# Optimization experiments

Hardware: AMD Instinct MI355X
Metric: run time of the kernel (lower is better)

The kernel has to match this reference:

```python
import jax, jax.numpy as jnp
import numpy as np

B, N, DIM, H = 8, 1024, 1024, 8
HEAD_DIM = DIM // H
SCALE = HEAD_DIM ** -0.5  # scale_with_head=True


def setup_inputs() -> dict:
    key = jax.random.key(0)
    k1, k2, k3, k4 = jax.random.split(key, 4)
    return {
        "q": jax.random.normal(k1, (B, N, DIM), dtype=jnp.float32),
        "k": jax.random.normal(k2, (B, N, DIM), dtype=jnp.float32),
        "v": jax.random.normal(k3, (B, N, DIM), dtype=jnp.float32),
        "W_out": jax.random.normal(k4, (DIM, DIM), dtype=jnp.float32) * (DIM ** -0.5),
        "b_out": jnp.zeros((DIM,), dtype=jnp.float32),
    }


def reference(q, k, v, W_out, b_out):
    b, n, dim = q.shape
    h, d = H, dim // H
    # b n (h d) -> b h n d
    def split_heads(t):
        return t.reshape(b, n, h, d).transpose(0, 2, 1, 3)
    qh, kh, vh = split_heads(q), split_heads(k), split_heads(v)
    dots = jnp.einsum('bhid,bhjd->bhij', qh, kh) * SCALE
    attn = jax.nn.softmax(dots, axis=-1)
    out = jnp.einsum('bhij,bhjd->bhid', attn, vh)
    out = out.transpose(0, 2, 1, 3).reshape(b, n, dim)  # b h n d -> b n (h d)
    out = out @ W_out.T + b_out  # nn.Linear(dim, dim); dropout p=0 is identity
    return out, attn
```

## Files before the change

kernel.cpp:

```cpp
#include <hip/hip_runtime.h>

typedef __bf16 bf16x8 __attribute__((ext_vector_type(8)));
typedef unsigned short u16x8 __attribute__((ext_vector_type(8)));
typedef unsigned short u16x4 __attribute__((ext_vector_type(4)));
typedef float f32x4 __attribute__((ext_vector_type(4)));
typedef float f32x16 __attribute__((ext_vector_type(16)));

#define B_    8
#define N_    1024
#define DIM_  1024
#define H_    8
#define HD_   128
#define SCALE_ 0.08838834764831845f

__device__ __forceinline__ unsigned short f2bf(float x) {
  unsigned int u = __float_as_uint(x);
  u += 0x7fffu + ((u >> 16) & 1u);
  return (unsigned short)(u >> 16);
}
__device__ __forceinline__ float bf2f(unsigned short h) {
  return __uint_as_float(((unsigned int)h) << 16);
}
__device__ __forceinline__ f32x4 mfma16(u16x8 a, u16x8 b, f32x4 c) {
  return __builtin_amdgcn_mfma_f32_16x16x32_bf16(
      __builtin_bit_cast(bf16x8, a), __builtin_bit_cast(bf16x8, b), c, 0, 0, 0);
}
__device__ __forceinline__ f32x16 mfma32(u16x8 a, u16x8 b, f32x16 c) {
  return __builtin_amdgcn_mfma_f32_32x32x16_bf16(
      __builtin_bit_cast(bf16x8, a), __builtin_bit_cast(bf16x8, b), c, 0, 0, 0);
}
__device__ __forceinline__ void gl_lds16(const void* g, void* l) {
  __builtin_amdgcn_global_load_lds(
      (const __attribute__((address_space(1))) unsigned int*)g,
      (__attribute__((address_space(3))) unsigned int*)l, 16, 0, 0);
}
#define SBAR() do { asm volatile("" ::: "memory"); __builtin_amdgcn_s_barrier(); \
                    asm volatile("" ::: "memory"); } while (0)
#define LGKM0() do { asm volatile("s_waitcnt lgkmcnt(0)" ::: "memory"); \
                     __builtin_amdgcn_sched_barrier(0); } while (0)
#define VMC(n)  asm volatile("s_waitcnt vmcnt(" #n ")" ::: "memory")

#define WS_KIMG  ((size_t)0)
#define WS_VIMG  ((size_t)32 << 20)
#define WS_WIMG  ((size_t)64 << 20)
#define WS_AOIMG ((size_t)68 << 20)

__global__ __launch_bounds__(256)
void prep_all(const float* __restrict__ gk, const float* __restrict__ gv,
              const float* __restrict__ gw, char* __restrict__ kimg,
              char* __restrict__ vimg, char* __restrict__ wimg) {
  const int blk = blockIdx.x;
  const int t = threadIdx.x;
  if (blk < 1024) {
    const int bh = blk >> 4, it = blk & 15;
    const int bb = bh >> 3, hh = bh & 7;
    char* base = kimg + (size_t)bh * 524288 + it * 32768;
    const float* src = gk + ((size_t)bb * N_ + it * 64) * DIM_ + hh * HD_;
    #pragma unroll
    for (int c = 0; c < 8; ++c) {
      const int idx = t + 256 * c;
      const int key = idx >> 5, dq = (idx & 31) * 4;
      f32x4 f = *(const f32x4*)(src + (size_t)key * DIM_ + dq);
      u16x4 h, g;
      #pragma unroll
      for (int j = 0; j < 4; ++j) {
        unsigned short hv = f2bf(f[j]);
        h[j] = hv;
        g[j] = f2bf(f[j] - bf2f(hv));
      }
      const int dh = dq >> 6, dloc = dq & 63;
      const int off = (dloc * 2) ^ ((key & 7) << 4);
      char* dst = base + dh * 16384 + key * 256;
      *(u16x4*)(dst + off) = h;
      *(u16x4*)(dst + 128 + off) = g;
    }
  } else if (blk < 3072) {
    __shared__ float tile[32][132];
    const int b2 = blk - 1024;
    const int bh = b2 >> 5, kt = b2 & 31;
    const int bb = bh >> 3, hh = bh & 7;
    const float* src = gv + ((size_t)bb * N_ + kt * 32) * DIM_ + hh * HD_;
    #pragma unroll
    for (int c = 0; c < 4; ++c) {
      const int idx = t + 256 * c;
      const int key = idx >> 5, dq = (idx & 31) * 4;
      *(f32x4*)&tile[key][dq] = *(const f32x4*)(src + (size_t)key * DIM_ + dq);
    }
    __syncthreads();
    char* base = vimg + (size_t)bh * 524288 + kt * 16384;
    #pragma unroll
    for (int c = 0; c < 2; ++c) {
      const int oc = t + 256 * c;
      const int d = oc >> 2, kc = oc & 3;
      u16x8 h, g;
      #pragma unroll
      for (int j = 0; j < 8; ++j) {
        float x = tile[kc * 8 + j][d];
        unsigned short hv = f2bf(x);
        h[j] = hv;
        g[j] = f2bf(x - bf2f(hv));
      }
      const int off = (d * 64 + kc * 16) ^ ((d & 7) << 4);
      *(u16x8*)(base + off) = h;
      *(u16x8*)(base + 8192 + off) = g;
    }
  } else {
    const int idx = (blk - 3072) * 256 + t;
    const int n = idx >> 7, k0 = (idx & 127) * 8;
    const float* s = gw + (size_t)n * DIM_ + k0;
    f32x4 f0 = *(const f32x4*)s;
    f32x4 f1 = *(const f32x4*)(s + 4);
    u16x8 h, g;
    #pragma unroll
    for (int j = 0; j < 8; ++j) {
      float x = j < 4 ? f0[j] : f1[j - 4];
      unsigned short hv = f2bf(x);
      h[j] = hv;
      g[j] = f2bf(x - bf2f(hv));
    }
    const int T = (n >> 7) * 32 + (k0 >> 5);
    const int rl = n & 127, kl = k0 & 31;
    char* base = wimg + (size_t)T * 16384 + rl * 128;
    const int swz = (rl & 7) << 4;
    *(u16x8*)(base + ((kl * 2) ^ swz)) = h;
    *(u16x8*)(base + ((64 + kl * 2) ^ swz)) = g;
  }
}

struct K1Smem {
  unsigned short p[64 * 1024];
  union {
    char kb[2][16384];
    char vt[2][16384];
    char comb[8][4096];
    struct { char pad[16384]; float partial[4][64]; float rinv[64]; } pp;
  } u;
};

__global__ __launch_bounds__(1024, 4)
void attn_kernel(const float* __restrict__ gq, const char* __restrict__ kimg,
                 const char* __restrict__ vimg, float* __restrict__ gattn,
                 char* __restrict__ aoimg) {
  __shared__ K1Smem sm;
  const int bid = blockIdx.x;
  const int xcd = bid & 7, slot = bid >> 3;
  const int bh = xcd + 8 * (slot >> 4);
  const int qt = slot & 15;
  const int bb = bh >> 3, hh = bh & 7;

  const int tid = threadIdx.x;
  const int wid = tid >> 6, lane = tid & 63;
  const int rg = wid >> 2;
  const int kg = wid & 3;
  const int l15 = lane & 15, l4 = lane >> 4;
  const int prg = wid >> 3;
  const int pkg = wid & 3;
  const int pkh = (wid >> 2) & 1;
  const int l31 = lane & 31, l5 = lane >> 5;

  const char* kimg_bh = kimg + (size_t)bh * 524288;
  const char* vimg_bh = vimg + (size_t)bh * 524288;

  auto issueK = [&](int s) {
    const char* src = kimg_bh + s * 16384 + wid * 1024 + lane * 16;
    gl_lds16(src, sm.u.kb[s & 1] + wid * 1024);
  };
  auto issueV = [&](int kt) {
    const char* src = vimg_bh + kt * 16384 + wid * 1024 + lane * 16;
    gl_lds16(src, sm.u.vt[kt & 1] + wid * 1024);
  };

  issueK(0);

  u16x8 qhi[4], qlo[4];
  {
    const int qrow = qt * 64 + rg * 16 + l15;
    const float* qp = gq + ((size_t)bb * N_ + qrow) * DIM_ + hh * HD_;
    #pragma unroll
    for (int t = 0; t < 4; ++t) {
      const int d0 = t * 32 + l4 * 8;
      f32x4 f0 = *(const f32x4*)(qp + d0);
      f32x4 f1 = *(const f32x4*)(qp + d0 + 4);
      #pragma unroll
      for (int j = 0; j < 8; ++j) {
        float x = (j < 4 ? f0[j] : f1[j - 4]) * SCALE_;
        unsigned short hi = f2bf(x);
        qhi[t][j] = hi;
        qlo[t][j] = f2bf(x - bf2f(hi));
      }
    }
  }

  issueK(1);
  VMC(1);
  SBAR();

  float lsum = 0.f;
  const int key16 = kg * 16 + l15;
  const int kswz = (key16 & 7) << 4;
  const char* krow0 = sm.u.kb[0] + key16 * 256;
  const char* krow1 = sm.u.kb[1] + key16 * 256;
  const int prow_i = rg * 16 + l15;
  char* const prow = (char*)sm.p + prow_i * 2048;
  const int pswz = (prow_i & 7) << 4;

  f32x4 a0, a1, a2;
  #pragma unroll 2
  for (int s = 0; s < 32; ++s) {
    const int dh = s & 1;
    if (s >= 1 && s < 31) issueK(s + 1);
    else if (s == 31) issueV(0);
    const char* krow = dh ? krow1 : krow0;
    u16x8 khi[2], klo[2];
    #pragma unroll
    for (int tl = 0; tl < 2; ++tl) {
      const int off = (tl * 64 + l4 * 16) ^ kswz;
      khi[tl] = *(const u16x8*)(krow + off);
      klo[tl] = *(const u16x8*)(krow + 128 + off);
    }
    if (dh == 0) {
      a0 = f32x4{0.f, 0.f, 0.f, 0.f};
      a1 = f32x4{0.f, 0.f, 0.f, 0.f};
      a2 = f32x4{0.f, 0.f, 0.f, 0.f};
    }
    __builtin_amdgcn_s_setprio(1);
    #pragma unroll
    for (int tl = 0; tl < 2; ++tl) {
      const int t = dh * 2 + tl;
      a0 = mfma16(khi[tl], qhi[t], a0);
      a1 = mfma16(klo[tl], qhi[t], a1);
      a2 = mfma16(khi[tl], qlo[t], a2);
    }
    __builtin_amdgcn_s_setprio(0);
    if (dh == 1) {
      const int keyb = ((s >> 1) * 64 + kg * 16 + l4 * 4) * 2;
      u16x4 pk;
      float ls = 0.f;
      #pragma unroll
      for (int r = 0; r < 4; ++r) {
        float sv = (a0[r] + a1[r]) + a2[r];
        sv = fminf(sv, 60.0f);
        float p = __expf(sv);
        ls += p;
        pk[r] = f2bf(p);
      }
      lsum += ls;
      *(u16x4*)(prow + (keyb ^ pswz)) = pk;
    }
    if (s < 31) { VMC(0); }
    else       { VMC(2); }
    SBAR();
  }

  {
    float s0 = lsum;
    s0 += __shfl_xor(s0, 16);
    s0 += __shfl_xor(s0, 32);
    if (lane < 16) sm.u.pp.partial[kg][rg * 16 + lane] = s0;
  }
  LGKM0();
  SBAR();
  if (tid < 64) {
    float t4 = sm.u.pp.partial[0][tid] + sm.u.pp.partial[1][tid] +
               sm.u.pp.partial[2][tid] + sm.u.pp.partial[3][tid];
    sm.u.pp.rinv[tid] = 1.0f / t4;
  }
  LGKM0();
  SBAR();
  const bool wr8 = (wid < 8);
  const int wrow = wid * 8 + (lane >> 3);
  const float rvs = sm.u.pp.rinv[wrow & 63];
  float rv16[16];
  if (pkh == 0) {
    #pragma unroll
    for (int r = 0; r < 16; ++r) {
      const int rowreg = (r & 3) + 8 * (r >> 2) + 4 * l5;
      rv16[r] = sm.u.pp.rinv[prg * 32 + rowreg];
    }
  }
  LGKM0();
  VMC(0);
  SBAR();

  f32x16 acc = {};
  const char* pArow = (const char*)sm.p + (prg * 32 + l31) * 2048;
  const int paswz = ((prg * 32 + l31) & 7) << 4;
  const char* wprow = (const char*)sm.p + wrow * 2048;
  const int wswz = (wrow & 7) << 4;
  float* wdst = gattn + ((size_t)bh * N_ + qt * 64 + wrow) * N_ + (lane & 7) * 4;
  const int dpv = pkg * 32 + l31;
  const int voff = (dpv * 64 + pkh * 32 + l5 * 16) ^ ((dpv & 7) << 4);

  #pragma unroll 2
  for (int kt = 0; kt < 32; ++kt) {
    if (kt < 31) issueV(kt + 1);
    const char* vbase = sm.u.vt[kt & 1];
    u16x8 vh = *(const u16x8*)(vbase + voff);
    u16x8 vl = *(const u16x8*)(vbase + 8192 + voff);
    u16x8 pa = *(const u16x8*)(pArow + ((kt * 64 + pkh * 32 + l5 * 16) ^ paswz));
    __builtin_amdgcn_s_setprio(1);
    acc = mfma32(pa, vh, acc);
    acc = mfma32(pa, vl, acc);
    __builtin_amdgcn_s_setprio(0);
    if (wr8) {
      u16x4 pw = *(const u16x4*)(wprow + ((kt * 64 + (lane & 7) * 8) ^ wswz));
      f32x4 o;
      o[0] = bf2f(pw[0]) * rvs; o[1] = bf2f(pw[1]) * rvs;
      o[2] = bf2f(pw[2]) * rvs; o[3] = bf2f(pw[3]) * rvs;
      __builtin_nontemporal_store(o, (f32x4*)(wdst + kt * 32));
    }
    LGKM0();
    if (kt < 31) {
      if (wr8) { VMC(1); }
      else     { VMC(0); }
    }
    SBAR();
  }

  {
    char* cbase = sm.u.comb[prg * 4 + pkg] + lane * 64;
    if (pkh == 1) {
      #pragma unroll
      for (int q = 0; q < 4; ++q) {
        f32x4 v = {acc[q * 4], acc[q * 4 + 1], acc[q * 4 + 2], acc[q * 4 + 3]};
        *(f32x4*)(cbase + q * 16) = v;
      }
    }
    LGKM0();
    SBAR();
    if (pkh == 0) {
      #pragma unroll
      for (int q = 0; q < 4; ++q) {
        f32x4 v = *(const f32x4*)(cbase + q * 16);
        acc[q * 4] += v[0]; acc[q * 4 + 1] += v[1];
        acc[q * 4 + 2] += v[2]; acc[q * 4 + 3] += v[3];
      }
      const int col5 = hh * 4 + pkg;
      const int mt = bb * 8 + (qt >> 1);
      char* Tbase = aoimg + ((size_t)(mt * 32 + col5)) * 16384;
      const int klb = l31 * 2;
      #pragma unroll
      for (int r = 0; r < 16; ++r) {
        const int rowreg = (r & 3) + 8 * (r >> 2) + 4 * l5;
        const int rl = (qt & 1) * 64 + prg * 32 + rowreg;
        const int swz = (rl & 7) << 4;
        float val = acc[r] * rv16[r];
        unsigned short hv = f2bf(val);
        unsigned short lv = f2bf(val - bf2f(hv));
        char* rp = Tbase + rl * 128;
        __builtin_nontemporal_store(hv, (unsigned short*)(rp + (klb ^ swz)));
        __builtin_nontemporal_store(lv, (unsigned short*)(rp + ((64 + klb) ^ swz)));
      }
    }
  }
}

struct K2Smem {
  char A[2][16384];
  char Bm[2][16384];
};

__global__ __launch_bounds__(512, 2)
void proj_kernel(const char* __restrict__ aoimg, const char* __restrict__ wimg,
                 const float* __restrict__ gbias, float* __restrict__ gout) {
  __shared__ K2Smem sm;
  const int nt = blockIdx.x & 7;
  const int mt = blockIdx.x >> 3;
  const int tid = threadIdx.x;
  const int wid = tid >> 6, lane = tid & 63;
  const int wr = wid >> 2, wc = wid & 3;
  const int l15 = lane & 15, l4 = lane >> 4;

  auto issue = [&](int s) {
    const char* sa = aoimg + ((size_t)(mt * 32 + s)) * 16384 + tid * 16;
    gl_lds16(sa, sm.A[s & 1] + (tid >> 6) * 1024);
    gl_lds16(sa + 8192, sm.A[s & 1] + 8192 + (tid >> 6) * 1024);
    const char* sb = wimg + ((size_t)(nt * 32 + s)) * 16384 + tid * 16;
    gl_lds16(sb, sm.Bm[s & 1] + (tid >> 6) * 1024);
    gl_lds16(sb + 8192, sm.Bm[s & 1] + 8192 + (tid >> 6) * 1024);
  };

  f32x4 acc[4][2];
  #pragma unroll
  for (int i = 0; i < 4; ++i)
    #pragma unroll
    for (int j = 0; j < 2; ++j) acc[i][j] = f32x4{0.f, 0.f, 0.f, 0.f};

  issue(0);
  VMC(0);
  SBAR();
  #pragma unroll 1
  for (int s = 0; s < 32; ++s) {
    if (s < 31) issue(s + 1);
    const char* Ab = sm.A[s & 1];
    const char* Bb = sm.Bm[s & 1];
    u16x8 ah[4], al[4], bh[2], bl[2];
    #pragma unroll
    for (int rt = 0; rt < 4; ++rt) {
      const int rl = wr * 64 + rt * 16 + l15;
      const char* rp = Ab + rl * 128;
      const int swz = (rl & 7) << 4;
      ah[rt] = *(const u16x8*)(rp + ((l4 * 16) ^ swz));
      al[rt] = *(const u16x8*)(rp + ((64 + l4 * 16) ^ swz));
    }
    #pragma unroll
    for (int ct = 0; ct < 2; ++ct) {
      const int cl = wc * 32 + ct * 16 + l15;
      const char* rp = Bb + cl * 128;
      const int swz = (cl & 7) << 4;
      bh[ct] = *(const u16x8*)(rp + ((l4 * 16) ^ swz));
      bl[ct] = *(const u16x8*)(rp + ((64 + l4 * 16) ^ swz));
    }
    __builtin_amdgcn_s_setprio(1);
    #pragma unroll
    for (int rt = 0; rt < 4; ++rt)
      #pragma unroll
      for (int ct = 0; ct < 2; ++ct)
        acc[rt][ct] = mfma16(ah[rt], bh[ct], acc[rt][ct]);
    #pragma unroll
    for (int rt = 0; rt < 4; ++rt)
      #pragma unroll
      for (int ct = 0; ct < 2; ++ct)
        acc[rt][ct] = mfma16(ah[rt], bl[ct], acc[rt][ct]);
    #pragma unroll
    for (int rt = 0; rt < 4; ++rt)
      #pragma unroll
      for (int ct = 0; ct < 2; ++ct)
        acc[rt][ct] = mfma16(al[rt], bh[ct], acc[rt][ct]);
    __builtin_amdgcn_s_setprio(0);
    LGKM0();
    if (s < 31) VMC(0);
    SBAR();
  }

  #pragma unroll
  for (int ct = 0; ct < 2; ++ct) {
    const int col = nt * 128 + wc * 32 + ct * 16 + l15;
    const float bv = gbias[col];
    #pragma unroll
    for (int rt = 0; rt < 4; ++rt) {
      float* dst = gout + (size_t)(mt * 128 + wr * 64 + rt * 16 + l4 * 4) * DIM_ + col;
      #pragma unroll
      for (int r = 0; r < 4; ++r)
        dst[(size_t)r * DIM_] = acc[rt][ct][r] + bv;
    }
  }
}

extern "C" void kernel_launch(void* const* d_in, const int* in_sizes, int n_in,
                              void* d_out, int out_size, void* d_ws, size_t ws_size,
                              hipStream_t stream) {
  const float* q    = (const float*)d_in[0];
  const float* k    = (const float*)d_in[1];
  const float* v    = (const float*)d_in[2];
  const float* W    = (const float*)d_in[3];
  const float* bias = (const float*)d_in[4];
  float* out  = (float*)d_out;
  float* attn = out + (size_t)B_ * N_ * DIM_;

  char* ws = (char*)d_ws;
  char* kimg  = ws + WS_KIMG;
  char* vimg  = ws + WS_VIMG;
  char* wimg  = ws + WS_WIMG;
  char* aoimg = ws + WS_AOIMG;

  prep_all<<<3584, 256, 0, stream>>>(k, v, W, kimg, vimg, wimg);
  attn_kernel<<<B_ * H_ * (N_ / 64), 1024, 0, stream>>>(q, kimg, vimg, attn, aoimg);
  proj_kernel<<<512, 512, 0, stream>>>(aoimg, wimg, bias, out);
}
```

Before: 243.4 us.

## Halve attention query tile to 32 rows, single-buffer K/V, use exp2 and packed bf16 convert

The attention kernel now handles 32 query rows per block with 512 threads instead of 64 rows with 1024. It replaces the double-buffered K/V LDS with a single buffer guarded by an extra barrier, which halves shared memory per block so more blocks can be resident. The softmax now folds log2(e) into the Q scale and uses v_exp_f32 plus v_cvt_pk_bf16_f32 to pack probabilities. The trade-off is an extra barrier per iteration, loads that no longer overlap compute, and twice as many K/V reads from global memory.

Result: slower. 294.4 us (+20.9%).

```diff
diff --git a/kernel.cpp b/kernel.cpp
--- a/kernel.cpp
+++ b/kernel.cpp
@@ -3,15 +3,17 @@
 typedef __bf16 bf16x8 __attribute__((ext_vector_type(8)));
 typedef unsigned short u16x8 __attribute__((ext_vector_type(8)));
 typedef unsigned short u16x4 __attribute__((ext_vector_type(4)));
+typedef float f32x2 __attribute__((ext_vector_type(2)));
 typedef float f32x4 __attribute__((ext_vector_type(4)));
 typedef float f32x16 __attribute__((ext_vector_type(16)));
+typedef unsigned int u32x2 __attribute__((ext_vector_type(2)));
 
 #define B_    8
 #define N_    1024
 #define DIM_  1024
 #define H_    8
 #define HD_   128
-#define SCALE_ 0.08838834764831845f
+#define SCALE2_ (0.08838834764831845f * 1.4426950408889634f)
 
 __device__ __forceinline__ unsigned short f2bf(float x) {
   unsigned int u = __float_as_uint(x);
@@ -33,6 +35,16 @@
   __builtin_amdgcn_global_load_lds(
       (const __attribute__((address_space(1))) unsigned int*)g,
       (__attribute__((address_space(3))) unsigned int*)l, 16, 0, 0);
+}
+__device__ __forceinline__ float exp2_hw(float x) {
+  float r;
+  asm("v_exp_f32 %0, %1" : "=v"(r) : "v"(x));
+  return r;
+}
+__device__ __forceinline__ unsigned int cvtpk_bf16(float lo, float hi) {
+  unsigned int r;
+  asm("v_cvt_pk_bf16_f32 %0, %1, %2" : "=v"(r) : "v"(lo), "v"(hi));
+  return r;
 }
 #define SBAR() do { asm volatile("" ::: "memory"); __builtin_amdgcn_s_barrier(); \
                     asm volatile("" ::: "memory"); } while (0)
@@ -52,10 +64,10 @@
   const int blk = blockIdx.x;
   const int t = threadIdx.x;
   if (blk < 1024) {
-    const int bh = blk >> 4, it = blk & 15;
+    const int bh = blk >> 4, tile = blk & 15;
     const int bb = bh >> 3, hh = bh & 7;
-    char* base = kimg + (size_t)bh * 524288 + it * 32768;
-    const float* src = gk + ((size_t)bb * N_ + it * 64) * DIM_ + hh * HD_;
+    char* base = kimg + (size_t)bh * 524288 + tile * 32768;
+    const float* src = gk + ((size_t)bb * N_ + tile * 64) * DIM_ + hh * HD_;
     #pragma unroll
     for (int c = 0; c < 8; ++c) {
       const int idx = t + 256 * c;
@@ -128,24 +140,23 @@
 }
 
 struct K1Smem {
-  unsigned short p[64 * 1024];
+  unsigned short p[32 * 1024];
   union {
-    char kb[2][16384];
-    char vt[2][16384];
-    char comb[8][4096];
-    struct { char pad[16384]; float partial[4][64]; float rinv[64]; } pp;
+    char kb[16384];
+    char vt[16384];
+    struct { float partial[4][32]; float rinv[32]; } pp;
   } u;
 };
 
-__global__ __launch_bounds__(1024, 4)
+__global__ __launch_bounds__(512, 4)
 void attn_kernel(const float* __restrict__ gq, const char* __restrict__ kimg,
                  const char* __restrict__ vimg, float* __restrict__ gattn,
                  char* __restrict__ aoimg) {
   __shared__ K1Smem sm;
   const int bid = blockIdx.x;
   const int xcd = bid & 7, slot = bid >> 3;
-  const int bh = xcd + 8 * (slot >> 4);
-  const int qt = slot & 15;
+  const int bh = xcd + 8 * (slot >> 5);
+  const int qt = slot & 31;
   const int bb = bh >> 3, hh = bh & 7;
 
   const int tid = threadIdx.x;
@@ -153,28 +164,31 @@
   const int rg = wid >> 2;
   const int kg = wid & 3;
   const int l15 = lane & 15, l4 = lane >> 4;
-  const int prg = wid >> 3;
   const int pkg = wid & 3;
-  const int pkh = (wid >> 2) & 1;
+  const int pkh = wid >> 2;
   const int l31 = lane & 31, l5 = lane >> 5;
 
   const char* kimg_bh = kimg + (size_t)bh * 524288;
   const char* vimg_bh = vimg + (size_t)bh * 524288;
 
   auto issueK = [&](int s) {
-    const char* src = kimg_bh + s * 16384 + wid * 1024 + lane * 16;
-    gl_lds16(src, sm.u.kb[s & 1] + wid * 1024);
+    const char* src = kimg_bh + s * 16384 + wid * 2048 + lane * 16;
+    char* dst = sm.u.kb + wid * 2048;
+    gl_lds16(src, dst);
+    gl_lds16(src + 1024, dst + 1024);
   };
   auto issueV = [&](int kt) {
-    const char* src = vimg_bh + kt * 16384 + wid * 1024 + lane * 16;
-    gl_lds16(src, sm.u.vt[kt & 1] + wid * 1024);
+    const char* src = vimg_bh + kt * 16384 + wid * 2048 + lane * 16;
+    char* dst = sm.u.vt + wid * 2048;
+    gl_lds16(src, dst);
+    gl_lds16(src + 1024, dst + 1024);
   };
 
   issueK(0);
 
   u16x8 qhi[4], qlo[4];
   {
-    const int qrow = qt * 64 + rg * 16 + l15;
+    const int qrow = qt * 32 + rg * 16 + l15;
     const float* qp = gq + ((size_t)bb * N_ + qrow) * DIM_ + hh * HD_;
     #pragma unroll
     for (int t = 0; t < 4; ++t) {
@@ -183,7 +197,7 @@
       f32x4 f1 = *(const f32x4*)(qp + d0 + 4);
       #pragma unroll
       for (int j = 0; j < 8; ++j) {
-        float x = (j < 4 ? f0[j] : f1[j - 4]) * SCALE_;
+        float x = (j < 4 ? f0[j] : f1[j - 4]) * SCALE2_;
         unsigned short hi = f2bf(x);
         qhi[t][j] = hi;
         qlo[t][j] = f2bf(x - bf2f(hi));
@@ -191,26 +205,22 @@
     }
   }
 
-  issueK(1);
-  VMC(1);
+  VMC(0);
   SBAR();
 
   float lsum = 0.f;
   const int key16 = kg * 16 + l15;
   const int kswz = (key16 & 7) << 4;
-  const char* krow0 = sm.u.kb[0] + key16 * 256;
-  const char* krow1 = sm.u.kb[1] + key16 * 256;
   const int prow_i = rg * 16 + l15;
   char* const prow = (char*)sm.p + prow_i * 2048;
   const int pswz = (prow_i & 7) << 4;
 
   f32x4 a0, a1, a2;
+  float sv0, sv1, sv2, sv3;
   #pragma unroll 2
   for (int s = 0; s < 32; ++s) {
     const int dh = s & 1;
-    if (s >= 1 && s < 31) issueK(s + 1);
-    else if (s == 31) issueV(0);
-    const char* krow = dh ? krow1 : krow0;
+    const char* krow = sm.u.kb + key16 * 256;
     u16x8 khi[2], klo[2];
     #pragma unroll
     for (int tl = 0; tl < 2; ++tl) {
@@ -233,22 +243,26 @@
     }
     __builtin_amdgcn_s_setprio(0);
     if (dh == 1) {
+      sv0 = (a0[0] + a1[0]) + a2[0];
+      sv1 = (a0[1] + a1[1]) + a2[1];
+      sv2 = (a0[2] + a1[2]) + a2[2];
+      sv3 = (a0[3] + a1[3]) + a2[3];
+    }
+    SBAR();
+    if (s < 31) issueK(s + 1);
+    if (dh == 1) {
+      float p0 = exp2_hw(fminf(sv0, 86.0f));
+      float p1 = exp2_hw(fminf(sv1, 86.0f));
+      float p2 = exp2_hw(fminf(sv2, 86.0f));
+      float p3 = exp2_hw(fminf(sv3, 86.0f));
+      lsum += (p0 + p1) + (p2 + p3);
+      u32x2 pk;
+      pk[0] = cvtpk_bf16(p0, p1);
+      pk[1] = cvtpk_bf16(p2, p3);
       const int keyb = ((s >> 1) * 64 + kg * 16 + l4 * 4) * 2;
-      u16x4 pk;
-      float ls = 0.f;
-      #pragma unroll
-      for (int r = 0; r < 4; ++r) {
-        float sv = (a0[r] + a1[r]) + a2[r];
-        sv = fminf(sv, 60.0f);
-        float p = __expf(sv);
-        ls += p;
-        pk[r] = f2bf(p);
-      }
-      lsum += ls;
-      *(u16x4*)(prow + (keyb ^ pswz)) = pk;
-    }
-    if (s < 31) { VMC(0); }
-    else       { VMC(2); }
+      *(u32x2*)(prow + (keyb ^ pswz)) = pk;
+    }
+    if (s < 31) VMC(0);
     SBAR();
   }
 
@@ -260,65 +274,63 @@
   }
   LGKM0();
   SBAR();
-  if (tid < 64) {
+  if (tid < 32) {
     float t4 = sm.u.pp.partial[0][tid] + sm.u.pp.partial[1][tid] +
                sm.u.pp.partial[2][tid] + sm.u.pp.partial[3][tid];
     sm.u.pp.rinv[tid] = 1.0f / t4;
   }
   LGKM0();
   SBAR();
-  const bool wr8 = (wid < 8);
-  const int wrow = wid * 8 + (lane >> 3);
-  const float rvs = sm.u.pp.rinv[wrow & 63];
+  const int wrow = wid * 4 + (lane >> 4);
+  const float rvs = sm.u.pp.rinv[wrow];
   float rv16[16];
   if (pkh == 0) {
     #pragma unroll
     for (int r = 0; r < 16; ++r) {
       const int rowreg = (r & 3) + 8 * (r >> 2) + 4 * l5;
-      rv16[r] = sm.u.pp.rinv[prg * 32 + rowreg];
+      rv16[r] = sm.u.pp.rinv[rowreg];
     }
   }
   LGKM0();
+  SBAR();
+  issueV(0);
   VMC(0);
   SBAR();
 
   f32x16 acc = {};
-  const char* pArow = (const char*)sm.p + (prg * 32 + l31) * 2048;
-  const int paswz = ((prg * 32 + l31) & 7) << 4;
+  const char* pArow = (const char*)sm.p + l31 * 2048;
+  const int paswz = (l31 & 7) << 4;
   const char* wprow = (const char*)sm.p + wrow * 2048;
   const int wswz = (wrow & 7) << 4;
-  float* wdst = gattn + ((size_t)bh * N_ + qt * 64 + wrow) * N_ + (lane & 7) * 4;
+  float* wdst = gattn + ((size_t)bh * N_ + qt * 32 + wrow) * N_ + (lane & 15) * 2;
   const int dpv = pkg * 32 + l31;
   const int voff = (dpv * 64 + pkh * 32 + l5 * 16) ^ ((dpv & 7) << 4);
 
   #pragma unroll 2
   for (int kt = 0; kt < 32; ++kt) {
-    if (kt < 31) issueV(kt + 1);
-    const char* vbase = sm.u.vt[kt & 1];
-    u16x8 vh = *(const u16x8*)(vbase + voff);
-    u16x8 vl = *(const u16x8*)(vbase + 8192 + voff);
+    u16x8 vh = *(const u16x8*)(sm.u.vt + voff);
+    u16x8 vl = *(const u16x8*)(sm.u.vt + 8192 + voff);
     u16x8 pa = *(const u16x8*)(pArow + ((kt * 64 + pkh * 32 + l5 * 16) ^ paswz));
     __builtin_amdgcn_s_setprio(1);
     acc = mfma32(pa, vh, acc);
     acc = mfma32(pa, vl, acc);
     __builtin_amdgcn_s_setprio(0);
-    if (wr8) {
-      u16x4 pw = *(const u16x4*)(wprow + ((kt * 64 + (lane & 7) * 8) ^ wswz));
-      f32x4 o;
-      o[0] = bf2f(pw[0]) * rvs; o[1] = bf2f(pw[1]) * rvs;
-      o[2] = bf2f(pw[2]) * rvs; o[3] = bf2f(pw[3]) * rvs;
-      __builtin_nontemporal_store(o, (f32x4*)(wdst + kt * 32));
-    }
-    LGKM0();
-    if (kt < 31) {
-      if (wr8) { VMC(1); }
-      else     { VMC(0); }
-    }
+    SBAR();
+    if (kt < 31) issueV(kt + 1);
+    {
+      unsigned int pw = *(const unsigned int*)
+          (wprow + ((kt * 64 + (lane & 15) * 4) ^ wswz));
+      f32x2 o;
+      o[0] = bf2f((unsigned short)(pw & 0xffffu)) * rvs;
+      o[1] = bf2f((unsigned short)(pw >> 16)) * rvs;
+      __builtin_nontemporal_store(o, (f32x2*)(wdst + kt * 32));
+    }
+    if (kt < 31) VMC(1);
     SBAR();
   }
 
   {
-    char* cbase = sm.u.comb[prg * 4 + pkg] + lane * 64;
+    char* cbase = (char*)sm.p + pkg * 8192 + lane * 64;
     if (pkh == 1) {
       #pragma unroll
       for (int q = 0; q < 4; ++q) {
@@ -336,13 +348,13 @@
         acc[q * 4 + 2] += v[2]; acc[q * 4 + 3] += v[3];
       }
       const int col5 = hh * 4 + pkg;
-      const int mt = bb * 8 + (qt >> 1);
+      const int mt = bb * 8 + (qt >> 2);
       char* Tbase = aoimg + ((size_t)(mt * 32 + col5)) * 16384;
       const int klb = l31 * 2;
       #pragma unroll
       for (int r = 0; r < 16; ++r) {
         const int rowreg = (r & 3) + 8 * (r >> 2) + 4 * l5;
-        const int rl = (qt & 1) * 64 + prg * 32 + rowreg;
+        const int rl = (qt & 3) * 32 + rowreg;
         const int swz = (rl & 7) << 4;
         float val = acc[r] * rv16[r];
         unsigned short hv = f2bf(val);
@@ -465,6 +477,6 @@
   char* aoimg = ws + WS_AOIMG;
 
   prep_all<<<3584, 256, 0, stream>>>(k, v, W, kimg, vimg, wimg);
-  attn_kernel<<<B_ * H_ * (N_ / 64), 1024, 0, stream>>>(q, kimg, vimg, attn, aoimg);
+  attn_kernel<<<B_ * H_ * (N_ / 32), 512, 0, stream>>>(q, kimg, vimg, attn, aoimg);
   proj_kernel<<<512, 512, 0, stream>>>(aoimg, wimg, bias, out);
 }
```
